# Optimization experiments

Hardware: AMD Instinct MI355X
Metric: run time of the kernel (lower is better)

The kernel has to match this reference:

```python
import jax, jax.numpy as jnp
import numpy as np

EPS = 1e-12  # F.normalize eps


def setup_inputs() -> dict:
    key = jax.random.key(0)
    k1, k2, k3 = jax.random.split(key, 3)
    N, C, H, W, K = 64, 512, 28, 28, 64
    x = jax.random.normal(k1, (N, C, H, W), dtype=jnp.float32)
    conv_w = jax.random.normal(k2, (K, C), dtype=jnp.float32)  # 1x1 conv weight squeezed
    centroids = jax.random.uniform(k3, (K, C), dtype=jnp.float32)  # torch.rand init
    return {"x": x, "conv_w": conv_w, "centroids": centroids}


def reference(x, conv_w, centroids):
    N, C, H, W = x.shape
    K = centroids.shape[0]
    xf = x.reshape(N, C, H * W)                                  # (N, C, L)
    # 1x1 conv == matmul over channels, softmax over cluster dim
    logits = jnp.einsum('kc,ncl->nkl', conv_w, xf)               # (N, K, L)
    a = jax.nn.softmax(logits, axis=1)                           # softmax over clusters
    # vlad[n,k,c] = sum_l a[n,k,l] * (x[n,c,l] - cent[k,c])
    #            = (a @ x^T)[n,k,c] - (sum_l a[n,k,l]) * cent[k,c]
    agg = jnp.einsum('nkl,ncl->nkc', a, xf)                      # (N, K, C)
    vlad = agg - a.sum(axis=-1)[..., None] * centroids[None]     # (N, K, C)
    # intra-normalize per cluster (dim=2)
    vlad = vlad / jnp.maximum(jnp.linalg.norm(vlad, axis=2, keepdims=True), EPS)
    v = vlad.reshape(N, K * C)
    # global L2 normalize
    v = v / jnp.maximum(jnp.linalg.norm(v, axis=1, keepdims=True), EPS)
    return v
```

## Files before the change

kernel.cpp:

```cpp
#include <hip/hip_runtime.h>

#define C_ 512
#define L_ 784
#define K_ 64
#define EPS_ 1e-12f

typedef _Float16 half_t;
typedef _Float16 half8 __attribute__((ext_vector_type(8)));
typedef float float4v __attribute__((ext_vector_type(4)));

__global__ __launch_bounds__(1024) void kF(const float* __restrict__ x,
                                           const float* __restrict__ w,
                                           float* __restrict__ aggP,
                                           float* __restrict__ asumP) {
    __shared__ half_t xt[16 * 520];
    __shared__ half_t xc[2][512 * 40];
    __shared__ float  sl[4 * 16 * 65];
    __shared__ half_t ah[64 * 40];

    const int t    = threadIdx.x;
    const int n    = blockIdx.y;
    const int bx   = blockIdx.x;
    const int l0   = bx * 192;
    const int NT   = (bx == 3) ? 13 : 12;
    const int wv   = t >> 6;
    const int lane = t & 63;
    const int m16  = lane & 15;
    const int q    = lane >> 4;
    const int kt   = wv & 3;
    const int cs   = wv >> 2;

    const float* xn = x + (size_t)n * (C_ * L_);

    half8 wf[4];
    {
        const float* wr = w + (size_t)(kt * 16 + m16) * C_ + cs * 128 + 8 * q;
#pragma unroll
        for (int st = 0; st < 4; ++st) {
            float4v f0 = *(const float4v*)(wr + 32 * st);
            float4v f1 = *(const float4v*)(wr + 32 * st + 4);
            wf[st] = half8{(half_t)f0.x, (half_t)f0.y, (half_t)f0.z, (half_t)f0.w,
                           (half_t)f1.x, (half_t)f1.y, (half_t)f1.z, (half_t)f1.w};
        }
    }

    const int sc  = t >> 1;
    const int slq = t & 1;
    const float* xs = xn + (size_t)sc * L_ + l0 + 8 * slq;

    {
        float4v f0 = *(const float4v*)xs;
        float4v f1 = *(const float4v*)(xs + 4);
        half8 h = {(half_t)f0.x, (half_t)f0.y, (half_t)f0.z, (half_t)f0.w,
                   (half_t)f1.x, (half_t)f1.y, (half_t)f1.z, (half_t)f1.w};
        *(half8*)&xc[0][sc * 40 + 8 * slq] = h;
#pragma unroll
        for (int j = 0; j < 8; ++j) xt[(8 * slq + j) * 520 + sc] = h[j];
    }

    float4v agc[8];
#pragma unroll
    for (int i = 0; i < 8; ++i) agc[i] = float4v{0.f, 0.f, 0.f, 0.f};
    float asum_reg = 0.f;

    __syncthreads();

    for (int s = 0; s < NT; ++s) {
        float4v p0, p1;
        const bool pf = (s + 1 < NT);
        if (pf) {
            const float* p = xs + (s + 1) * 16;
            p0 = *(const float4v*)p;
            p1 = *(const float4v*)(p + 4);
        }
        {
            float4v lac = {0.f, 0.f, 0.f, 0.f};
#pragma unroll
            for (int st = 0; st < 4; ++st) {
                half8 A = *(const half8*)&xt[m16 * 520 + cs * 128 + st * 32 + 8 * q];
                lac = __builtin_amdgcn_mfma_f32_16x16x32_f16(A, wf[st], lac, 0, 0, 0);
            }
#pragma unroll
            for (int r = 0; r < 4; ++r)
                sl[cs * 1040 + (4 * q + r) * 65 + kt * 16 + m16] = lac[r];
        }
        __syncthreads();
        {
            float lg = sl[wv * 65 + lane] + sl[1040 + wv * 65 + lane] +
                       sl[2080 + wv * 65 + lane] + sl[3120 + wv * 65 + lane];
            float mx = lg;
#pragma unroll
            for (int off = 32; off; off >>= 1) mx = fmaxf(mx, __shfl_xor(mx, off, 64));
            float e = __expf(lg - mx);
            float sm = e;
#pragma unroll
            for (int off = 32; off; off >>= 1) sm += __shfl_xor(sm, off, 64);
            float a = e / sm;
            asum_reg += a;
            ah[lane * 40 + (s & 1) * 16 + wv] = (half_t)a;
        }
        if (pf) {
            half8 h = {(half_t)p0.x, (half_t)p0.y, (half_t)p0.z, (half_t)p0.w,
                       (half_t)p1.x, (half_t)p1.y, (half_t)p1.z, (half_t)p1.w};
            const int sp = s + 1;
            *(half8*)&xc[(sp >> 1) & 1][sc * 40 + (sp & 1) * 16 + 8 * slq] = h;
#pragma unroll
            for (int j = 0; j < 8; ++j) xt[(8 * slq + j) * 520 + sc] = h[j];
        }
        __syncthreads();
        const bool tail_single = (s == NT - 1) && !(s & 1);
        if (tail_single) {
            ah[(t >> 4) * 40 + 16 + (t & 15)] = (half_t)0.f;
            __syncthreads();
        }
        if ((s & 1) || tail_single) {
            const half_t* xcb = xc[(s >> 1) & 1];
            half8 A = *(const half8*)&ah[(kt * 16 + m16) * 40 + 8 * q];
#pragma unroll
            for (int i = 0; i < 8; ++i) {
                half8 B = *(const half8*)&xcb[((cs * 8 + i) * 16 + m16) * 40 + 8 * q];
                agc[i] = __builtin_amdgcn_mfma_f32_16x16x32_f16(A, B, agc[i], 0, 0, 0);
            }
        }
    }

    sl[wv * 64 + lane] = asum_reg;
    __syncthreads();
    if (t < 64) {
        float s_ = 0.f;
#pragma unroll
        for (int j = 0; j < 16; ++j) s_ += sl[j * 64 + t];
        asumP[((size_t)n * 4 + bx) * 64 + t] = s_;
    }
    float* ap = aggP + (((size_t)n * 4 + bx) * 64) * (size_t)C_;
#pragma unroll
    for (int i = 0; i < 8; ++i)
#pragma unroll
        for (int r = 0; r < 4; ++r)
            ap[(size_t)(kt * 16 + 4 * q + r) * C_ + (cs * 8 + i) * 16 + m16] = agc[i][r];
}

__global__ __launch_bounds__(256) void kC(const float* __restrict__ aggP,
                                          const float* __restrict__ cent,
                                          const float* __restrict__ asumP,
                                          float* __restrict__ out) {
    __shared__ float asumS[8];
    const int t  = threadIdx.x;
    const int n  = blockIdx.y;
    const int k0 = blockIdx.x * 8;
    if (t < 8) {
        float s = 0.f;
        for (int j = 0; j < 4; ++j) s += asumP[((size_t)n * 4 + j) * 64 + k0 + t];
        asumS[t] = s;
    }
    __syncthreads();
    const int wv   = t >> 6;
    const int lane = t & 63;
    for (int r = wv; r < 8; r += 4) {
        const int k = k0 + r;
        const float as = asumS[r];
        const float* a0 = aggP + (((size_t)n * 4 + 0) * 64 + k) * C_;
        const float* a1 = aggP + (((size_t)n * 4 + 1) * 64 + k) * C_;
        const float* a2 = aggP + (((size_t)n * 4 + 2) * 64 + k) * C_;
        const float* a3 = aggP + (((size_t)n * 4 + 3) * 64 + k) * C_;
        const float* cp = cent + (size_t)k * C_;
        float v[8];
        float ss = 0.f;
#pragma unroll
        for (int j = 0; j < 8; ++j) {
            const int c = lane + 64 * j;
            float val = a0[c] + a1[c] + a2[c] + a3[c] - as * cp[c];
            v[j] = val;
            ss += val * val;
        }
#pragma unroll
        for (int off = 32; off; off >>= 1) ss += __shfl_xor(ss, off, 64);
        const float scale = 1.f / (fmaxf(sqrtf(ss), EPS_) * 8.f);
        float* op = out + (size_t)n * (K_ * C_) + (size_t)k * C_;
#pragma unroll
        for (int j = 0; j < 8; ++j) op[lane + 64 * j] = v[j] * scale;
    }
}

extern "C" void kernel_launch(void* const* d_in, const int* in_sizes, int n_in,
                              void* d_out, int out_size, void* d_ws, size_t ws_size,
                              hipStream_t stream) {
    (void)in_sizes; (void)n_in; (void)out_size; (void)ws_size;
    const float* x    = (const float*)d_in[0];
    const float* w    = (const float*)d_in[1];
    const float* cent = (const float*)d_in[2];
    float* out = (float*)d_out;

    char* base = (char*)d_ws;
    float* aggP  = (float*)base;
    float* asumP = aggP + (size_t)64 * 4 * 64 * 512;

    kF<<<dim3(4, 64), 1024, 0, stream>>>(x, w, aggP, asumP);
    kC<<<dim3(8, 64), 256, 0, stream>>>(aggP, cent, asumP, out);
}
```

Before: 183.3 us.

## Load x tiles directly into registers and transpose via identity MFMA

Drops the LDS staging buffers for x (both transposed and chunked copies). Each wave now loads its own x fragment from global memory into registers and builds the transposed operand by multiplying with an identity matrix through MFMA. The aggregation MFMA then runs every step with 16x16x16 instead of batching two steps. The change removes most LDS traffic and a barrier, which should allow higher occupancy (launch bounds raised to 4 blocks), at the cost of extra MFMAs, losing the software prefetch, and strided uncoalesced global loads. The finalize kernel is also switched to float4 vector loads and stores.

```diff
diff --git a/kernel.cpp b/kernel.cpp
--- a/kernel.cpp
+++ b/kernel.cpp
@@ -6,17 +6,15 @@
 #define EPS_ 1e-12f
 
 typedef _Float16 half_t;
-typedef _Float16 half8 __attribute__((ext_vector_type(8)));
+typedef _Float16 half4 __attribute__((ext_vector_type(4)));
 typedef float float4v __attribute__((ext_vector_type(4)));
 
-__global__ __launch_bounds__(1024) void kF(const float* __restrict__ x,
-                                           const float* __restrict__ w,
-                                           float* __restrict__ aggP,
-                                           float* __restrict__ asumP) {
-    __shared__ half_t xt[16 * 520];
-    __shared__ half_t xc[2][512 * 40];
-    __shared__ float  sl[4 * 16 * 65];
-    __shared__ half_t ah[64 * 40];
+__global__ __launch_bounds__(1024, 4) void kF(const float* __restrict__ x,
+                                              const float* __restrict__ w,
+                                              float* __restrict__ aggP,
+                                              float* __restrict__ asumP) {
+    __shared__ float  sl[16 * 64 * 4];
+    __shared__ half_t ah[64 * 20];
 
     const int t    = threadIdx.x;
     const int n    = blockIdx.y;
@@ -32,62 +30,46 @@
 
     const float* xn = x + (size_t)n * (C_ * L_);
 
-    half8 wf[4];
-    {
-        const float* wr = w + (size_t)(kt * 16 + m16) * C_ + cs * 128 + 8 * q;
+    half4 wf[8];
 #pragma unroll
-        for (int st = 0; st < 4; ++st) {
-            float4v f0 = *(const float4v*)(wr + 32 * st);
-            float4v f1 = *(const float4v*)(wr + 32 * st + 4);
-            wf[st] = half8{(half_t)f0.x, (half_t)f0.y, (half_t)f0.z, (half_t)f0.w,
-                           (half_t)f1.x, (half_t)f1.y, (half_t)f1.z, (half_t)f1.w};
-        }
+    for (int i = 0; i < 8; ++i) {
+        float4v f = *(const float4v*)(w + (size_t)(kt * 16 + m16) * C_ +
+                                      cs * 128 + i * 16 + 4 * q);
+        wf[i] = half4{(half_t)f[0], (half_t)f[1], (half_t)f[2], (half_t)f[3]};
     }
+    half4 ifr;
+#pragma unroll
+    for (int j = 0; j < 4; ++j) ifr[j] = (half_t)((4 * q + j == m16) ? 1.0f : 0.0f);
 
-    const int sc  = t >> 1;
-    const int slq = t & 1;
-    const float* xs = xn + (size_t)sc * L_ + l0 + 8 * slq;
-
-    {
-        float4v f0 = *(const float4v*)xs;
-        float4v f1 = *(const float4v*)(xs + 4);
-        half8 h = {(half_t)f0.x, (half_t)f0.y, (half_t)f0.z, (half_t)f0.w,
-                   (half_t)f1.x, (half_t)f1.y, (half_t)f1.z, (half_t)f1.w};
-        *(half8*)&xc[0][sc * 40 + 8 * slq] = h;
-#pragma unroll
-        for (int j = 0; j < 8; ++j) xt[(8 * slq + j) * 520 + sc] = h[j];
-    }
-
+    const float4v z4 = {0.f, 0.f, 0.f, 0.f};
     float4v agc[8];
 #pragma unroll
-    for (int i = 0; i < 8; ++i) agc[i] = float4v{0.f, 0.f, 0.f, 0.f};
+    for (int i = 0; i < 8; ++i) agc[i] = z4;
     float asum_reg = 0.f;
 
-    __syncthreads();
-
     for (int s = 0; s < NT; ++s) {
-        float4v p0, p1;
-        const bool pf = (s + 1 < NT);
-        if (pf) {
-            const float* p = xs + (s + 1) * 16;
-            p0 = *(const float4v*)p;
-            p1 = *(const float4v*)(p + 4);
+        const int ls = l0 + 16 * s;
+        half4 bh[8];
+        float4v lac0 = z4, lac1 = z4;
+#pragma unroll
+        for (int i = 0; i < 8; ++i) {
+            float4v xq = *(const float4v*)(xn + (size_t)((cs * 8 + i) * 16 + m16) * L_ +
+                                           ls + 4 * q);
+            half4 s4 = {(half_t)xq[0], (half_t)xq[1], (half_t)xq[2], (half_t)xq[3]};
+            bh[i] = s4;
+            float4v xt = __builtin_amdgcn_mfma_f32_16x16x16f16(s4, ifr, z4, 0, 0, 0);
+            half4 a4 = {(half_t)xt[0], (half_t)xt[1], (half_t)xt[2], (half_t)xt[3]};
+            if (i < 4) lac0 = __builtin_amdgcn_mfma_f32_16x16x16f16(a4, wf[i], lac0, 0, 0, 0);
+            else       lac1 = __builtin_amdgcn_mfma_f32_16x16x16f16(a4, wf[i], lac1, 0, 0, 0);
         }
-        {
-            float4v lac = {0.f, 0.f, 0.f, 0.f};
+        float4v lac = lac0 + lac1;
 #pragma unroll
-            for (int st = 0; st < 4; ++st) {
-                half8 A = *(const half8*)&xt[m16 * 520 + cs * 128 + st * 32 + 8 * q];
-                lac = __builtin_amdgcn_mfma_f32_16x16x32_f16(A, wf[st], lac, 0, 0, 0);
-            }
-#pragma unroll
-            for (int r = 0; r < 4; ++r)
-                sl[cs * 1040 + (4 * q + r) * 65 + kt * 16 + m16] = lac[r];
-        }
+        for (int r = 0; r < 4; ++r)
+            sl[((4 * q + r) * 64 + kt * 16 + m16) * 4 + cs] = lac[r];
         __syncthreads();
         {
-            float lg = sl[wv * 65 + lane] + sl[1040 + wv * 65 + lane] +
-                       sl[2080 + wv * 65 + lane] + sl[3120 + wv * 65 + lane];
+            float4v p4 = *(const float4v*)&sl[(wv * 64 + lane) * 4];
+            float lg = p4[0] + p4[1] + p4[2] + p4[3];
             float mx = lg;
 #pragma unroll
             for (int off = 32; off; off >>= 1) mx = fmaxf(mx, __shfl_xor(mx, off, 64));
@@ -97,31 +79,13 @@
             for (int off = 32; off; off >>= 1) sm += __shfl_xor(sm, off, 64);
             float a = e / sm;
             asum_reg += a;
-            ah[lane * 40 + (s & 1) * 16 + wv] = (half_t)a;
-        }
-        if (pf) {
-            half8 h = {(half_t)p0.x, (half_t)p0.y, (half_t)p0.z, (half_t)p0.w,
-                       (half_t)p1.x, (half_t)p1.y, (half_t)p1.z, (half_t)p1.w};
-            const int sp = s + 1;
-            *(half8*)&xc[(sp >> 1) & 1][sc * 40 + (sp & 1) * 16 + 8 * slq] = h;
-#pragma unroll
-            for (int j = 0; j < 8; ++j) xt[(8 * slq + j) * 520 + sc] = h[j];
+            ah[lane * 20 + wv] = (half_t)a;
         }
         __syncthreads();
-        const bool tail_single = (s == NT - 1) && !(s & 1);
-        if (tail_single) {
-            ah[(t >> 4) * 40 + 16 + (t & 15)] = (half_t)0.f;
-            __syncthreads();
-        }
-        if ((s & 1) || tail_single) {
-            const half_t* xcb = xc[(s >> 1) & 1];
-            half8 A = *(const half8*)&ah[(kt * 16 + m16) * 40 + 8 * q];
+        half4 aA = *(const half4*)&ah[(kt * 16 + m16) * 20 + 4 * q];
 #pragma unroll
-            for (int i = 0; i < 8; ++i) {
-                half8 B = *(const half8*)&xcb[((cs * 8 + i) * 16 + m16) * 40 + 8 * q];
-                agc[i] = __builtin_amdgcn_mfma_f32_16x16x32_f16(A, B, agc[i], 0, 0, 0);
-            }
-        }
+        for (int i = 0; i < 8; ++i)
+            agc[i] = __builtin_amdgcn_mfma_f32_16x16x16f16(aA, bh[i], agc[i], 0, 0, 0);
     }
 
     sl[wv * 64 + lane] = asum_reg;
@@ -164,21 +128,34 @@
         const float* a2 = aggP + (((size_t)n * 4 + 2) * 64 + k) * C_;
         const float* a3 = aggP + (((size_t)n * 4 + 3) * 64 + k) * C_;
         const float* cp = cent + (size_t)k * C_;
-        float v[8];
+        float4v v[2];
         float ss = 0.f;
 #pragma unroll
-        for (int j = 0; j < 8; ++j) {
-            const int c = lane + 64 * j;
-            float val = a0[c] + a1[c] + a2[c] + a3[c] - as * cp[c];
+        for (int j = 0; j < 2; ++j) {
+            const int c = 4 * lane + 256 * j;
+            float4v val = *(const float4v*)(a0 + c);
+            val = val + *(const float4v*)(a1 + c);
+            val = val + *(const float4v*)(a2 + c);
+            val = val + *(const float4v*)(a3 + c);
+            float4v c4 = *(const float4v*)(cp + c);
+#pragma unroll
+            for (int e = 0; e < 4; ++e) {
+                val[e] -= as * c4[e];
+                ss += val[e] * val[e];
+            }
             v[j] = val;
-            ss += val * val;
         }
 #pragma unroll
         for (int off = 32; off; off >>= 1) ss += __shfl_xor(ss, off, 64);
         const float scale = 1.f / (fmaxf(sqrtf(ss), EPS_) * 8.f);
         float* op = out + (size_t)n * (K_ * C_) + (size_t)k * C_;
 #pragma unroll
-        for (int j = 0; j < 8; ++j) op[lane + 64 * j] = v[j] * scale;
+        for (int j = 0; j < 2; ++j) {
+            float4v o = v[j];
+#pragma unroll
+            for (int e = 0; e < 4; ++e) o[e] *= scale;
+            *(float4v*)(op + 4 * lane + 256 * j) = o;
+        }
     }
 }
 
```

Result: slower. 218.4 us (+19.2%).
